# Optimization experiments

Hardware: AMD Instinct MI355X
Metric: run time of the kernel (lower is better)

## Reference

```python
import jax, jax.numpy as jnp
import numpy as np

D = 1024
N = 50000
SCALE = 1.0 / D  # scale torch.rand-style params to keep exp() in range


def _attention_module(X, W_alpha, a_alpha, b_alpha, W_sum):
    # a_w, b_w: [1, D] row vectors (a_alpha.T @ W_alpha)
    a_w = a_alpha[:, 0] @ W_alpha  # [D]
    b_w = b_alpha[:, 0] @ W_alpha  # [D]
    # score_j = a_w . X[0] + b_w . X[j]  -> alpha_j = exp(score_j)
    scores = jnp.dot(a_w, X[0]) + X @ b_w  # [N]
    alpha = jnp.exp(scores)  # [N]
    # weighted sum over neighbors, normalized by total alpha
    sum_output = (alpha @ X) / jnp.sum(alpha)  # [D]
    return sum_output @ W_sum  # [D]


def setup_inputs() -> dict:
    key = jax.random.key(0)
    ks = jax.random.split(key, 12)
    rand = lambda k, shape: jax.random.uniform(k, shape, dtype=jnp.float32) * SCALE
    return {
        "X_in": jax.random.normal(ks[0], (N, D), dtype=jnp.float32),
        "X_out": jax.random.normal(ks[1], (N, D), dtype=jnp.float32),
        "W_alpha_in": rand(ks[2], (D, D)),
        "a_alpha_in": rand(ks[3], (D, 1)),
        "b_alpha_in": rand(ks[4], (D, 1)),
        "W_sum_in": rand(ks[5], (D, D)),
        "W_alpha_out": rand(ks[6], (D, D)),
        "a_alpha_out": rand(ks[7], (D, 1)),
        "b_alpha_out": rand(ks[8], (D, 1)),
        "W_sum_out": rand(ks[9], (D, D)),
        "lin_W": jax.random.normal(ks[10], (D, 2 * D), dtype=jnp.float32) / np.sqrt(2 * D),
        "lin_b": jnp.zeros((D,), dtype=jnp.float32),
    }


def reference(X_in, X_out, W_alpha_in, a_alpha_in, b_alpha_in, W_sum_in,
              W_alpha_out, a_alpha_out, b_alpha_out, W_sum_out, lin_W, lin_b):
    res_in = _attention_module(X_in, W_alpha_in, a_alpha_in, b_alpha_in, W_sum_in)    # [D]
    res_out = _attention_module(X_out, W_alpha_out, a_alpha_out, b_alpha_out, W_sum_out)  # [D]
    attn = jnp.concatenate([res_in, res_out], axis=0)  # [2D]
    return jax.nn.elu(attn @ lin_W.T + lin_b)  # [D]
```

## Files before the change

kernel.cpp:

```cpp
#include <hip/hip_runtime.h>
#include <math.h>


#define DD 1024
#define NROWS 50000
#define GB 512

__global__ __launch_bounds__(256) void vecmat_partial(
    const float* __restrict__ v0, const float* __restrict__ M0,
    const float* __restrict__ v1, const float* __restrict__ M1,
    float* __restrict__ out) {
  int bid = blockIdx.x;
  int module = bid >> 6;
  int r = bid & 63;
  int jb = r & 3;
  int ic = r >> 2;
  const float* __restrict__ v = module ? v1 : v0;
  const float* __restrict__ M = module ? M1 : M0;
  int j = jb * 256 + threadIdx.x;
  int i0 = ic * 64;
  float acc = 0.f;
#pragma unroll 4
  for (int i = i0; i < i0 + 64; ++i)
    acc = fmaf(v[i], M[i * DD + j], acc);
  atomicAdd(&out[module * DD + j], acc);
}

__global__ __launch_bounds__(256) void attn_pass(
    const float* __restrict__ X0, const float* __restrict__ X1,
    const float* __restrict__ bw_all,
    float* __restrict__ num0, float* __restrict__ den0,
    float* __restrict__ num1, float* __restrict__ den1) {
  int bid = blockIdx.x;
  int module = (bid >= GB) ? 1 : 0;
  int b = module ? bid - GB : bid;
  const float* __restrict__ X = module ? X1 : X0;
  float* __restrict__ num = module ? num1 : num0;
  float* __restrict__ den = module ? den1 : den0;
  const float* __restrict__ bw = bw_all + module * DD;

  int tid = threadIdx.x;
  int lane = tid & 63;
  int wave = tid >> 6;
  int w = b * 4 + wave;
  const int WPM = GB * 4;

  float4 bwv[4], acc[4];
#pragma unroll
  for (int q = 0; q < 4; ++q) {
    bwv[q] = *reinterpret_cast<const float4*>(&bw[q * 256 + lane * 4]);
    acc[q] = make_float4(0.f, 0.f, 0.f, 0.f);
  }
  float asum = 0.f;

  for (int j = w; j < NROWS; j += WPM) {
    const float4* __restrict__ row =
        reinterpret_cast<const float4*>(X + (size_t)j * DD);
    float4 xv[4];
#pragma unroll
    for (int q = 0; q < 4; ++q) xv[q] = row[q * 64 + lane];
    float s = 0.f;
#pragma unroll
    for (int q = 0; q < 4; ++q) {
      s = fmaf(xv[q].x, bwv[q].x, s);
      s = fmaf(xv[q].y, bwv[q].y, s);
      s = fmaf(xv[q].z, bwv[q].z, s);
      s = fmaf(xv[q].w, bwv[q].w, s);
    }
#pragma unroll
    for (int off = 32; off >= 1; off >>= 1) s += __shfl_xor(s, off, 64);
    float alpha = expf(s);
    asum += alpha;
#pragma unroll
    for (int q = 0; q < 4; ++q) {
      acc[q].x = fmaf(alpha, xv[q].x, acc[q].x);
      acc[q].y = fmaf(alpha, xv[q].y, acc[q].y);
      acc[q].z = fmaf(alpha, xv[q].z, acc[q].z);
      acc[q].w = fmaf(alpha, xv[q].w, acc[q].w);
    }
  }

  __shared__ float sdata[4][DD];
  __shared__ float dsum[4];
#pragma unroll
  for (int q = 0; q < 4; ++q)
    *reinterpret_cast<float4*>(&sdata[wave][q * 256 + lane * 4]) = acc[q];
  if (lane == 0) dsum[wave] = asum;
  __syncthreads();

  float4 a0 = *reinterpret_cast<float4*>(&sdata[0][tid * 4]);
  float4 a1 = *reinterpret_cast<float4*>(&sdata[1][tid * 4]);
  float4 a2 = *reinterpret_cast<float4*>(&sdata[2][tid * 4]);
  float4 a3 = *reinterpret_cast<float4*>(&sdata[3][tid * 4]);
  int c = tid * 4;
  atomicAdd(&num[c + 0], a0.x + a1.x + a2.x + a3.x);
  atomicAdd(&num[c + 1], a0.y + a1.y + a2.y + a3.y);
  atomicAdd(&num[c + 2], a0.z + a1.z + a2.z + a3.z);
  atomicAdd(&num[c + 3], a0.w + a1.w + a2.w + a3.w);
  if (tid == 0) atomicAdd(den, dsum[0] + dsum[1] + dsum[2] + dsum[3]);
}

__global__ __launch_bounds__(256) void final_kernel(
    const float* __restrict__ res_raw,
    const float* __restrict__ den0, const float* __restrict__ den1,
    const float* __restrict__ linW, const float* __restrict__ linb,
    float* __restrict__ out) {
  int k = blockIdx.x;
  int tid = threadIdx.x;
  float inv0 = 1.f / (*den0);
  float inv1 = 1.f / (*den1);
  const float* __restrict__ row = linW + (size_t)k * (2 * DD);
  float acc = 0.f;
#pragma unroll
  for (int s = 0; s < 8; ++s) {
    int m = s * 256 + tid;
    float attn = res_raw[m] * (m < DD ? inv0 : inv1);
    acc = fmaf(attn, row[m], acc);
  }
#pragma unroll
  for (int off = 32; off >= 1; off >>= 1) acc += __shfl_xor(acc, off, 64);
  __shared__ float wsum[4];
  int lane = tid & 63, wave = tid >> 6;
  if (lane == 0) wsum[wave] = acc;
  __syncthreads();
  if (tid == 0) {
    float v = wsum[0] + wsum[1] + wsum[2] + wsum[3] + linb[k];
    out[k] = v > 0.f ? v : expm1f(v);
  }
}

extern "C" void kernel_launch(void* const* d_in, const int* in_sizes, int n_in,
                              void* d_out, int out_size, void* d_ws, size_t ws_size,
                              hipStream_t stream) {
  const float* X_in    = (const float*)d_in[0];
  const float* X_out   = (const float*)d_in[1];
  const float* W_a_in  = (const float*)d_in[2];
  const float* b_a_in  = (const float*)d_in[4];
  const float* W_s_in  = (const float*)d_in[5];
  const float* W_a_out = (const float*)d_in[6];
  const float* b_a_out = (const float*)d_in[8];
  const float* W_s_out = (const float*)d_in[9];
  const float* linW    = (const float*)d_in[10];
  const float* linb    = (const float*)d_in[11];
  float* out = (float*)d_out;
  float* ws  = (float*)d_ws;

  float* bw      = ws;
  float* num0    = ws + 2048;
  float* den0    = ws + 3072;
  float* num1    = ws + 3073;
  float* den1    = ws + 4097;
  float* res_raw = ws + 4098;

  hipMemsetAsync(d_ws, 0, 6146 * sizeof(float), stream);
  vecmat_partial<<<128, 256, 0, stream>>>(b_a_in, W_a_in, b_a_out, W_a_out, bw);
  attn_pass<<<2 * GB, 256, 0, stream>>>(X_in, X_out, bw, num0, den0, num1, den1);
  vecmat_partial<<<128, 256, 0, stream>>>(num0, W_s_in, num1, W_s_out, res_raw);
  final_kernel<<<DD, 256, 0, stream>>>(res_raw, den0, den1, linW, linb, out);
}
```

Before: 487.2 us.

## Batch four rows per wave, spread atomics over partial buffers, widen vecmat grid

Result: faster. 447.7 us (-8.1%).

```diff
diff --git a/kernel.cpp b/kernel.cpp
--- a/kernel.cpp
+++ b/kernel.cpp
@@ -5,38 +5,38 @@
 #define DD 1024
 #define NROWS 50000
 #define GB 512
+#define RB 4
+#define NPART 16
 
 __global__ __launch_bounds__(256) void vecmat_partial(
     const float* __restrict__ v0, const float* __restrict__ M0,
     const float* __restrict__ v1, const float* __restrict__ M1,
     float* __restrict__ out) {
   int bid = blockIdx.x;
-  int module = bid >> 6;
-  int r = bid & 63;
+  int module = bid >> 7;
+  int r = bid & 127;
   int jb = r & 3;
   int ic = r >> 2;
   const float* __restrict__ v = module ? v1 : v0;
   const float* __restrict__ M = module ? M1 : M0;
   int j = jb * 256 + threadIdx.x;
-  int i0 = ic * 64;
+  int i0 = ic * 32;
   float acc = 0.f;
-#pragma unroll 4
-  for (int i = i0; i < i0 + 64; ++i)
+#pragma unroll 8
+  for (int i = i0; i < i0 + 32; ++i)
     acc = fmaf(v[i], M[i * DD + j], acc);
   atomicAdd(&out[module * DD + j], acc);
 }
 
-__global__ __launch_bounds__(256) void attn_pass(
+__global__ __launch_bounds__(256, 4) void attn_pass(
     const float* __restrict__ X0, const float* __restrict__ X1,
     const float* __restrict__ bw_all,
-    float* __restrict__ num0, float* __restrict__ den0,
-    float* __restrict__ num1, float* __restrict__ den1) {
+    float* __restrict__ num_part,
+    float* __restrict__ den_part) {
   int bid = blockIdx.x;
   int module = (bid >= GB) ? 1 : 0;
   int b = module ? bid - GB : bid;
   const float* __restrict__ X = module ? X1 : X0;
-  float* __restrict__ num = module ? num1 : num0;
-  float* __restrict__ den = module ? den1 : den0;
   const float* __restrict__ bw = bw_all + module * DD;
 
   int tid = threadIdx.x;
@@ -53,30 +53,44 @@
   }
   float asum = 0.f;
 
-  for (int j = w; j < NROWS; j += WPM) {
-    const float4* __restrict__ row =
-        reinterpret_cast<const float4*>(X + (size_t)j * DD);
-    float4 xv[4];
+  for (int j0 = w * RB; j0 < NROWS; j0 += WPM * RB) {
+    float4 xv[RB][4];
 #pragma unroll
-    for (int q = 0; q < 4; ++q) xv[q] = row[q * 64 + lane];
-    float s = 0.f;
+    for (int r = 0; r < RB; ++r) {
+      const float4* __restrict__ row =
+          reinterpret_cast<const float4*>(X + (size_t)(j0 + r) * DD);
 #pragma unroll
-    for (int q = 0; q < 4; ++q) {
-      s = fmaf(xv[q].x, bwv[q].x, s);
-      s = fmaf(xv[q].y, bwv[q].y, s);
-      s = fmaf(xv[q].z, bwv[q].z, s);
-      s = fmaf(xv[q].w, bwv[q].w, s);
+      for (int q = 0; q < 4; ++q) xv[r][q] = row[q * 64 + lane];
+    }
+    float s[RB];
+#pragma unroll
+    for (int r = 0; r < RB; ++r) {
+      float t = 0.f;
+#pragma unroll
+      for (int q = 0; q < 4; ++q) {
+        t = fmaf(xv[r][q].x, bwv[q].x, t);
+        t = fmaf(xv[r][q].y, bwv[q].y, t);
+        t = fmaf(xv[r][q].z, bwv[q].z, t);
+        t = fmaf(xv[r][q].w, bwv[q].w, t);
+      }
+      s[r] = t;
     }
 #pragma unroll
-    for (int off = 32; off >= 1; off >>= 1) s += __shfl_xor(s, off, 64);
-    float alpha = expf(s);
-    asum += alpha;
+    for (int off = 32; off >= 1; off >>= 1) {
 #pragma unroll
-    for (int q = 0; q < 4; ++q) {
-      acc[q].x = fmaf(alpha, xv[q].x, acc[q].x);
-      acc[q].y = fmaf(alpha, xv[q].y, acc[q].y);
-      acc[q].z = fmaf(alpha, xv[q].z, acc[q].z);
-      acc[q].w = fmaf(alpha, xv[q].w, acc[q].w);
+      for (int r = 0; r < RB; ++r) s[r] += __shfl_xor(s[r], off, 64);
+    }
+#pragma unroll
+    for (int r = 0; r < RB; ++r) {
+      float alpha = __expf(s[r]);
+      asum += alpha;
+#pragma unroll
+      for (int q = 0; q < 4; ++q) {
+        acc[q].x = fmaf(alpha, xv[r][q].x, acc[q].x);
+        acc[q].y = fmaf(alpha, xv[r][q].y, acc[q].y);
+        acc[q].z = fmaf(alpha, xv[r][q].z, acc[q].z);
+        acc[q].w = fmaf(alpha, xv[r][q].w, acc[q].w);
+      }
     }
   }
 
@@ -92,23 +106,43 @@
   float4 a1 = *reinterpret_cast<float4*>(&sdata[1][tid * 4]);
   float4 a2 = *reinterpret_cast<float4*>(&sdata[2][tid * 4]);
   float4 a3 = *reinterpret_cast<float4*>(&sdata[3][tid * 4]);
+  int p = module * NPART + (b & (NPART - 1));
+  float* __restrict__ np = num_part + (size_t)p * DD;
   int c = tid * 4;
-  atomicAdd(&num[c + 0], a0.x + a1.x + a2.x + a3.x);
-  atomicAdd(&num[c + 1], a0.y + a1.y + a2.y + a3.y);
-  atomicAdd(&num[c + 2], a0.z + a1.z + a2.z + a3.z);
-  atomicAdd(&num[c + 3], a0.w + a1.w + a2.w + a3.w);
-  if (tid == 0) atomicAdd(den, dsum[0] + dsum[1] + dsum[2] + dsum[3]);
+  atomicAdd(&np[c + 0], a0.x + a1.x + a2.x + a3.x);
+  atomicAdd(&np[c + 1], a0.y + a1.y + a2.y + a3.y);
+  atomicAdd(&np[c + 2], a0.z + a1.z + a2.z + a3.z);
+  atomicAdd(&np[c + 3], a0.w + a1.w + a2.w + a3.w);
+  if (tid == 0) atomicAdd(&den_part[p], dsum[0] + dsum[1] + dsum[2] + dsum[3]);
+}
+
+__global__ __launch_bounds__(256) void reduce_partials(
+    const float* __restrict__ num_part, const float* __restrict__ den_part,
+    float* __restrict__ num, float* __restrict__ den) {
+  int idx = blockIdx.x * 256 + threadIdx.x;
+  int m = idx >> 10;
+  int i = idx & (DD - 1);
+  float s = 0.f;
+#pragma unroll
+  for (int p = 0; p < NPART; ++p)
+    s += num_part[((size_t)(m * NPART + p)) * DD + i];
+  num[idx] = s;
+  if (idx < 2) {
+    float d = 0.f;
+#pragma unroll
+    for (int p = 0; p < NPART; ++p) d += den_part[idx * NPART + p];
+    den[idx] = d;
+  }
 }
 
 __global__ __launch_bounds__(256) void final_kernel(
-    const float* __restrict__ res_raw,
-    const float* __restrict__ den0, const float* __restrict__ den1,
+    const float* __restrict__ res_raw, const float* __restrict__ den,
     const float* __restrict__ linW, const float* __restrict__ linb,
     float* __restrict__ out) {
   int k = blockIdx.x;
   int tid = threadIdx.x;
-  float inv0 = 1.f / (*den0);
-  float inv1 = 1.f / (*den1);
+  float inv0 = 1.f / den[0];
+  float inv1 = 1.f / den[1];
   const float* __restrict__ row = linW + (size_t)k * (2 * DD);
   float acc = 0.f;
 #pragma unroll
@@ -145,16 +179,17 @@
   float* out = (float*)d_out;
   float* ws  = (float*)d_ws;
 
-  float* bw      = ws;
-  float* num0    = ws + 2048;
-  float* den0    = ws + 3072;
-  float* num1    = ws + 3073;
-  float* den1    = ws + 4097;
-  float* res_raw = ws + 4098;
+  float* bw       = ws;
+  float* num_part = ws + 2048;
+  float* den_part = ws + 34816;
+  float* num      = ws + 34848;
+  float* den      = ws + 36896;
+  float* res_raw  = ws + 36898;
 
-  hipMemsetAsync(d_ws, 0, 6146 * sizeof(float), stream);
-  vecmat_partial<<<128, 256, 0, stream>>>(b_a_in, W_a_in, b_a_out, W_a_out, bw);
-  attn_pass<<<2 * GB, 256, 0, stream>>>(X_in, X_out, bw, num0, den0, num1, den1);
-  vecmat_partial<<<128, 256, 0, stream>>>(num0, W_s_in, num1, W_s_out, res_raw);
-  final_kernel<<<DD, 256, 0, stream>>>(res_raw, den0, den1, linW, linb, out);
+  hipMemsetAsync(d_ws, 0, 38946 * sizeof(float), stream);
+  vecmat_partial<<<256, 256, 0, stream>>>(b_a_in, W_a_in, b_a_out, W_a_out, bw);
+  attn_pass<<<2 * GB, 256, 0, stream>>>(X_in, X_out, bw, num_part, den_part);
+  reduce_partials<<<8, 256, 0, stream>>>(num_part, den_part, num, den);
+  vecmat_partial<<<256, 256, 0, stream>>>(num, W_s_in, num + 1024, W_s_out, res_raw);
+  final_kernel<<<DD, 256, 0, stream>>>(res_raw, den, linW, linb, out);
 }
```
